# Kernel optimization log

Hardware: AMD Instinct MI355X
Metric: run time of the kernel (lower is better)

Reference implementation:

```python
import jax, jax.numpy as jnp
import numpy as np

B = 256
N = 256


def setup_inputs() -> dict:
    key = jax.random.key(0)
    ks = jax.random.split(key, 6)
    X = jax.random.normal(ks[0], (B, N), dtype=jnp.float32)
    context = jax.random.normal(ks[1], (B, N), dtype=jnp.float32)
    W = jax.random.normal(ks[2], (N, N), dtype=jnp.float32) * 0.1
    scale = jnp.ones((1,), dtype=jnp.float32)
    A = jax.random.uniform(ks[3], (N, N), dtype=jnp.float32)
    cl_weight = jax.random.normal(ks[4], (N * N, N), dtype=jnp.float32) * 0.02
    cl_bias = jax.random.normal(ks[5], (N * N,), dtype=jnp.float32) * 0.02
    t = 3
    return {"X": X, "context": context, "W": W, "scale": scale, "A": A,
            "cl_weight": cl_weight, "cl_bias": cl_bias, "t": t}


def reference(X, context, W, scale, A, cl_weight, cl_bias, t):
    # context_L path: context-conditioned adjustment of W, shape [B, N, N]
    Bsz, n = X.shape
    adjust = (context @ cl_weight.T + cl_bias).reshape(Bsz, n, n)
    W_new = adjust + W  # broadcast [N,N] over batch
    # diag term: sum over rows i of (W_new @ A)[b, i, k] = einsum bij,jk->bk
    d = jnp.einsum('bij,jk->bk', W_new, A)
    eye = jnp.eye(n, dtype=X.dtype)
    L = d[:, :, None] * eye - W_new          # diag_embed(d) - W_new, [B,N,N]
    new_context = context * (t / (t + 1)) + X / (t + 1)
    L_T = scale * jnp.swapaxes(L, -1, -2)    # [B,N,N]
    update = jnp.einsum('bn,bnm->bm', X, L_T)  # matmul(X[...,None,:], L_T).squeeze()
    return (update, new_context)
```

## Files before the change

kernel.cpp:

```cpp
#include <hip/hip_runtime.h>

#define N 256
#define NN 65536

typedef __attribute__((ext_vector_type(8))) __bf16 bf16x8;
typedef __attribute__((ext_vector_type(4))) __bf16 bf16x4v;
typedef __attribute__((ext_vector_type(4))) float f32x4;

#define F_PART   0u
#define F_SPART  2097152u
#define F_WSC    2621440u
#define F_WXCB   2621696u
#define F_SFULL  2687232u
#define F_YADJ   2752768u
#define F_CTXB   2818304u
#define WS_FLOATS 2851072u

static __device__ __forceinline__ f32x4 mfma16(bf16x8 a, bf16x8 b, f32x4 c) {
  return __builtin_amdgcn_mfma_f32_16x16x32_bf16(a, b, c, 0, 0, 0);
}
static __device__ __forceinline__ bf16x4v pack4(float4 v) {
  bf16x4v r;
  r[0] = (__bf16)v.x; r[1] = (__bf16)v.y; r[2] = (__bf16)v.z; r[3] = (__bf16)v.w;
  return r;
}

__global__ void __launch_bounds__(256) kpre(
    const float* __restrict__ X, const float* __restrict__ ctx,
    const float* __restrict__ W, const float* __restrict__ clb,
    const int* __restrict__ tptr, float* __restrict__ out,
    float* __restrict__ ws)
{
  extern __shared__ char smem[];
  const int blk = blockIdx.x;
  const int t = threadIdx.x;
  if (blk < 16) {
    const int b0 = (blk >> 2) * 64;
    const int m0 = (blk & 3) * 64;
    {
      const int row = t >> 2, q = t & 3;
      const int sw = (row & 7) << 4;
      const float4* xp = (const float4*)X + (b0 + row) * 64 + q * 16;
      const float4* wp = (const float4*)W + (m0 + row) * 64 + q * 16;
      const float4* cp = (const float4*)clb + (m0 + row) * 64 + q * 16;
      char* xs = smem;
      char* ps = smem + 32768;
#pragma unroll
      for (int i = 0; i < 16; ++i) {
        float4 xv = xp[i];
        *(bf16x4v*)(xs + row * 512 + ((q * 128 + i * 8) ^ sw)) = pack4(xv);
        float4 wv = wp[i];
        float4 cv = cp[i];
        float4 sv;
        sv.x = wv.x + cv.x; sv.y = wv.y + cv.y;
        sv.z = wv.z + cv.z; sv.w = wv.w + cv.w;
        *(bf16x4v*)(ps + row * 512 + ((q * 128 + i * 8) ^ sw)) = pack4(sv);
      }
    }
    __syncthreads();
    const int lane = t & 63, w = t >> 6;
    const int l15 = lane & 15, lhi = lane >> 4;
    const int wbl = (w >> 1) * 32, wml = (w & 1) * 32;
    const int swz = (l15 & 7) << 4;
    const f32x4 zero = {0.f, 0.f, 0.f, 0.f};
    f32x4 acc[2][2];
    acc[0][0] = zero; acc[0][1] = zero; acc[1][0] = zero; acc[1][1] = zero;
#pragma unroll
    for (int ks = 0; ks < 8; ++ks) {
      const int kb = ks * 64 + lhi * 16;
      bf16x8 a0 = *(const bf16x8*)(smem + (wbl + l15) * 512 + (kb ^ swz));
      bf16x8 a1 = *(const bf16x8*)(smem + (wbl + 16 + l15) * 512 + (kb ^ swz));
      bf16x8 b0 = *(const bf16x8*)(smem + 32768 + (wml + l15) * 512 + (kb ^ swz));
      bf16x8 b1 = *(const bf16x8*)(smem + 32768 + (wml + 16 + l15) * 512 + (kb ^ swz));
      acc[0][0] = mfma16(a0, b0, acc[0][0]);
      acc[0][1] = mfma16(a0, b1, acc[0][1]);
      acc[1][0] = mfma16(a1, b0, acc[1][0]);
      acc[1][1] = mfma16(a1, b1, acc[1][1]);
    }
#pragma unroll
    for (int fb = 0; fb < 2; ++fb)
#pragma unroll
      for (int fm = 0; fm < 2; ++fm)
#pragma unroll
        for (int r = 0; r < 4; ++r) {
          const int b = b0 + wbl + fb * 16 + lhi * 4 + r;
          const int m = m0 + wml + fm * 16 + l15;
          ws[F_WXCB + b * N + m] = acc[fb][fm][r];
        }
  } else if (blk == 16) {
    float sv = 0.f;
    for (int i = 0; i < N; ++i) sv += W[i * N + t] + clb[i * N + t];
    ws[F_WSC + t] = sv;
  } else if (blk < 81) {
    const float tf = (float)(*tptr);
    const float c1 = tf / (tf + 1.f);
    const float c2 = 1.f / (tf + 1.f);
    const int i4 = (blk - 17) * 256 + t;
    const float4 cv = ((const float4*)ctx)[i4];
    const float4 xv = ((const float4*)X)[i4];
    float4 o;
    o.x = cv.x * c1 + xv.x * c2;
    o.y = cv.y * c1 + xv.y * c2;
    o.z = cv.z * c1 + xv.z * c2;
    o.w = cv.w * c1 + xv.w * c2;
    ((float4*)out)[16384 + i4] = o;
  } else {
    const int g = (blk - 81) * 256 + t;
    const float4* p = (const float4*)ctx + g * 2;
    const float4 v0 = p[0], v1 = p[1];
    bf16x8 r;
    r[0] = (__bf16)v0.x; r[1] = (__bf16)v0.y; r[2] = (__bf16)v0.z; r[3] = (__bf16)v0.w;
    r[4] = (__bf16)v1.x; r[5] = (__bf16)v1.y; r[6] = (__bf16)v1.z; r[7] = (__bf16)v1.w;
    ((bf16x8*)(ws + F_CTXB))[g] = r;
  }
}

__global__ void __launch_bounds__(512) kbig(
    const float* __restrict__ X, const float* __restrict__ clw,
    float* __restrict__ ws)
{
  extern __shared__ char smem[];
  char* clws = smem + 131072;
  float* xl = (float*)(smem + 147456);
  const int t = threadIdx.x;
  const int mt = blockIdx.x >> 5;
  const int s = blockIdx.x & 31;
  const int n0 = s * 8;
  const int m0g = mt * 32;
  const float4* clwf4 = (const float4*)clw;

  float4 g0[4];
  int gm[4], gk[4];
#pragma unroll
  for (int i = 0; i < 4; ++i) {
    const int idx = i * 512 + t;
    gm[i] = idx >> 6;
    gk[i] = idx & 63;
    g0[i] = clwf4[(m0g + gm[i]) * 16384 + n0 * 64 + gk[i]];
  }
  {
    const bf16x8* cb = (const bf16x8*)(ws + F_CTXB);
#pragma unroll
    for (int it = 0; it < 16; ++it) {
      const int gg = it * 512 + t;
      bf16x8 v = cb[gg];
      const int row = gg >> 5, c8 = gg & 31;
      *(bf16x8*)(smem + row * 512 + ((c8 * 16) ^ ((row & 7) << 4))) = v;
    }
  }
  if (t < 256) {
    const float4* xp = (const float4*)(X + t * N + n0);
    const float4 x0 = xp[0], x1 = xp[1];
    xl[0 * N + t] = x0.x; xl[1 * N + t] = x0.y; xl[2 * N + t] = x0.z; xl[3 * N + t] = x0.w;
    xl[4 * N + t] = x1.x; xl[5 * N + t] = x1.y; xl[6 * N + t] = x1.z; xl[7 * N + t] = x1.w;
  }
#pragma unroll
  for (int i = 0; i < 4; ++i) {
    *(bf16x4v*)(clws + gm[i] * 512 + ((gk[i] * 8) ^ ((gm[i] & 7) << 4))) = pack4(g0[i]);
  }
  __syncthreads();

  const int lane = t & 63, w = t >> 6;
  const int wb = w * 32, l15 = lane & 15, lhi = lane >> 4;
  const int swz = (l15 & 7) << 4;
  const f32x4 zero = {0.f, 0.f, 0.f, 0.f};
  f32x4 acc[2][2];
  acc[0][0] = zero; acc[0][1] = zero; acc[1][0] = zero; acc[1][1] = zero;

  for (int nn = 0; nn < 8; ++nn) {
    float4 gnx[4];
    if (nn < 7) {
#pragma unroll
      for (int i = 0; i < 4; ++i)
        gnx[i] = clwf4[(m0g + gm[i]) * 16384 + (n0 + nn + 1) * 64 + gk[i]];
    }
    f32x4 h[2][2];
    h[0][0] = zero; h[0][1] = zero; h[1][0] = zero; h[1][1] = zero;
#pragma unroll
    for (int half = 0; half < 2; ++half) {
      bf16x8 af[2][4], bw[2][4];
#pragma unroll
      for (int q = 0; q < 4; ++q) {
        const int kb = half * 256 + q * 64 + lhi * 16;
        af[0][q] = *(const bf16x8*)(smem + (wb + l15) * 512 + (kb ^ swz));
        af[1][q] = *(const bf16x8*)(smem + (wb + 16 + l15) * 512 + (kb ^ swz));
        bw[0][q] = *(const bf16x8*)(clws + (l15) * 512 + (kb ^ swz));
        bw[1][q] = *(const bf16x8*)(clws + (16 + l15) * 512 + (kb ^ swz));
      }
#pragma unroll
      for (int q = 0; q < 4; ++q) {
        h[0][0] = mfma16(af[0][q], bw[0][q], h[0][0]);
        h[0][1] = mfma16(af[0][q], bw[1][q], h[0][1]);
        h[1][0] = mfma16(af[1][q], bw[0][q], h[1][0]);
        h[1][1] = mfma16(af[1][q], bw[1][q], h[1][1]);
      }
    }
    const int ng = n0 + nn;
#pragma unroll
    for (int fb = 0; fb < 2; ++fb) {
      float xv[4];
#pragma unroll
      for (int r = 0; r < 4; ++r)
        xv[r] = xl[nn * N + wb + fb * 16 + lhi * 4 + r];
#pragma unroll
      for (int r = 0; r < 4; ++r) {
        acc[fb][0][r] += xv[r] * h[fb][0][r];
        acc[fb][1][r] += xv[r] * h[fb][1][r];
        float v = h[fb][0][r] + h[fb][1][r];
        v += __shfl_xor(v, 1);
        v += __shfl_xor(v, 2);
        v += __shfl_xor(v, 4);
        v += __shfl_xor(v, 8);
        if (l15 == 0)
          ws[F_SPART + mt * NN + (wb + fb * 16 + lhi * 4 + r) * N + ng] = v;
      }
    }
    __syncthreads();
    if (nn < 7) {
#pragma unroll
      for (int i = 0; i < 4; ++i)
        *(bf16x4v*)(clws + gm[i] * 512 + ((gk[i] * 8) ^ ((gm[i] & 7) << 4))) = pack4(gnx[i]);
    }
    __syncthreads();
  }
  const int base = blockIdx.x * 8192;
#pragma unroll
  for (int fb = 0; fb < 2; ++fb)
#pragma unroll
    for (int fm = 0; fm < 2; ++fm)
#pragma unroll
      for (int r = 0; r < 4; ++r) {
        const int b = wb + fb * 16 + lhi * 4 + r;
        const int ml = fm * 16 + l15;
        ws[F_PART + base + b * 32 + ml] = acc[fb][fm][r];
      }
}

__global__ void __launch_bounds__(256) kred(float* __restrict__ ws)
{
  const int o = blockIdx.x * 256 + threadIdx.x;
  const int b = o >> 8, col = o & 255;
  const int mt = col >> 5, ml = col & 31;
  float y = 0.f;
#pragma unroll
  for (int si = 0; si < 32; ++si)
    y += ws[F_PART + ((mt * 32 + si) * 256 + b) * 32 + ml];
  ws[F_YADJ + o] = y;
  float sv = ws[F_WSC + col];
#pragma unroll
  for (int q = 0; q < 8; ++q)
    sv += ws[F_SPART + q * NN + o];
  ws[F_SFULL + o] = sv;
}

__global__ void __launch_bounds__(256) kfin(
    const float* __restrict__ X, const float* __restrict__ A,
    const float* __restrict__ scale, float* __restrict__ out,
    float* __restrict__ ws)
{
  extern __shared__ char smem[];
  const int t = threadIdx.x, blk = blockIdx.x;
  const int b0 = (blk >> 2) * 64, k0 = (blk & 3) * 64;
  {
    const int row = t >> 2, q = t & 3;
    const int sw = (row & 7) << 4;
    const float4* sp = (const float4*)(ws + F_SFULL + (b0 + row) * N) + q * 16;
#pragma unroll
    for (int i = 0; i < 16; ++i) {
      float4 v = sp[i];
      *(bf16x4v*)(smem + row * 512 + ((q * 128 + i * 8) ^ sw)) = pack4(v);
    }
  }
  {
    const int j = t;
    const float4* ap = (const float4*)(A + j * N + k0);
    char* at = smem + 32768;
#pragma unroll
    for (int i = 0; i < 16; ++i) {
      float4 v = ap[i];
      const int kk = i * 4;
      *(__bf16*)(at + (kk + 0) * 512 + ((j * 2) ^ (((kk + 0) & 7) << 4))) = (__bf16)v.x;
      *(__bf16*)(at + (kk + 1) * 512 + ((j * 2) ^ (((kk + 1) & 7) << 4))) = (__bf16)v.y;
      *(__bf16*)(at + (kk + 2) * 512 + ((j * 2) ^ (((kk + 2) & 7) << 4))) = (__bf16)v.z;
      *(__bf16*)(at + (kk + 3) * 512 + ((j * 2) ^ (((kk + 3) & 7) << 4))) = (__bf16)v.w;
    }
  }
  __syncthreads();
  const int lane = t & 63, w = t >> 6;
  const int l15 = lane & 15, lhi = lane >> 4;
  const int wbl = (w >> 1) * 32, wkl = (w & 1) * 32;
  const int swz = (l15 & 7) << 4;
  const f32x4 zero = {0.f, 0.f, 0.f, 0.f};
  f32x4 acc[2][2];
  acc[0][0] = zero; acc[0][1] = zero; acc[1][0] = zero; acc[1][1] = zero;
#pragma unroll
  for (int ks = 0; ks < 8; ++ks) {
    const int kb = ks * 64 + lhi * 16;
    bf16x8 a0 = *(const bf16x8*)(smem + (wbl + l15) * 512 + (kb ^ swz));
    bf16x8 a1 = *(const bf16x8*)(smem + (wbl + 16 + l15) * 512 + (kb ^ swz));
    bf16x8 b0 = *(const bf16x8*)(smem + 32768 + (wkl + l15) * 512 + (kb ^ swz));
    bf16x8 b1 = *(const bf16x8*)(smem + 32768 + (wkl + 16 + l15) * 512 + (kb ^ swz));
    acc[0][0] = mfma16(a0, b0, acc[0][0]);
    acc[0][1] = mfma16(a0, b1, acc[0][1]);
    acc[1][0] = mfma16(a1, b0, acc[1][0]);
    acc[1][1] = mfma16(a1, b1, acc[1][1]);
  }
  const float sc = scale[0];
#pragma unroll
  for (int fb = 0; fb < 2; ++fb)
#pragma unroll
    for (int fm = 0; fm < 2; ++fm)
#pragma unroll
      for (int r = 0; r < 4; ++r) {
        const int b = b0 + wbl + fb * 16 + lhi * 4 + r;
        const int k = k0 + wkl + fm * 16 + l15;
        const int idx = b * N + k;
        const float d = acc[fb][fm][r];
        out[idx] = sc * (X[idx] * d - ws[F_WXCB + idx] - ws[F_YADJ + idx]);
      }
}

extern "C" void kernel_launch(void* const* d_in, const int* in_sizes, int n_in,
                              void* d_out, int out_size, void* d_ws, size_t ws_size,
                              hipStream_t stream)
{
  const float* X     = (const float*)d_in[0];
  const float* ctx   = (const float*)d_in[1];
  const float* W     = (const float*)d_in[2];
  const float* scale = (const float*)d_in[3];
  const float* A     = (const float*)d_in[4];
  const float* clw   = (const float*)d_in[5];
  const float* clb   = (const float*)d_in[6];
  const int*   tptr  = (const int*)d_in[7];
  float* out = (float*)d_out;
  float* ws  = (float*)d_ws;

  if (ws_size < (size_t)WS_FLOATS * sizeof(float)) return;

  (void)hipFuncSetAttribute((const void*)kpre,
                            hipFuncAttributeMaxDynamicSharedMemorySize, 65536);
  (void)hipFuncSetAttribute((const void*)kbig,
                            hipFuncAttributeMaxDynamicSharedMemorySize, 155648);
  (void)hipFuncSetAttribute((const void*)kfin,
                            hipFuncAttributeMaxDynamicSharedMemorySize, 65536);

  kpre<<<113, 256, 65536, stream>>>(X, ctx, W, clb, tptr, out, ws);
  kbig<<<256, 512, 155648, stream>>>(X, clw, ws);
  kred<<<256, 256, 0, stream>>>(ws);
  kfin<<<16, 256, 65536, stream>>>(X, A, scale, out, ws);
}
```

Before: 61.35 us.

## Remove pre-pass kernel by fusing its work into main and final kernels

Deletes the kpre launch. Its jobs move elsewhere: kbig converts the ctx bf16 A-fragments straight into registers, kfin computes the X·(W+clb)ᵀ product and new_context, and the column sums of W+clb are produced by the mt==0 blocks of kbig. kbig shrinks its shared memory from about 152KB to 56KB by keeping the ctx operand in registers, and it triple-buffers the cl_weight slices with a two-step prefetch, using a single barrier per step. kfin is retiled from 16 to 64 blocks. The intent is to cut launch overhead and the workspace round trip and to raise occupancy, at the cost of more register pressure and redundant ctx loads across blocks.

```diff
diff --git a/kernel.cpp b/kernel.cpp
--- a/kernel.cpp
+++ b/kernel.cpp
@@ -10,11 +10,9 @@
 #define F_PART   0u
 #define F_SPART  2097152u
 #define F_WSC    2621440u
-#define F_WXCB   2621696u
-#define F_SFULL  2687232u
-#define F_YADJ   2752768u
-#define F_CTXB   2818304u
-#define WS_FLOATS 2851072u
+#define F_SFULL  2621696u
+#define F_YADJ   2687232u
+#define WS_FLOATS 2752768u
 
 static __device__ __forceinline__ f32x4 mfma16(bf16x8 a, bf16x8 b, f32x4 c) {
   return __builtin_amdgcn_mfma_f32_16x16x32_bf16(a, b, c, 0, 0, 0);
@@ -24,130 +22,51 @@
   r[0] = (__bf16)v.x; r[1] = (__bf16)v.y; r[2] = (__bf16)v.z; r[3] = (__bf16)v.w;
   return r;
 }
-
-__global__ void __launch_bounds__(256) kpre(
+static __device__ __forceinline__ bf16x8 pack8(float4 a, float4 b) {
+  bf16x8 r;
+  r[0] = (__bf16)a.x; r[1] = (__bf16)a.y; r[2] = (__bf16)a.z; r[3] = (__bf16)a.w;
+  r[4] = (__bf16)b.x; r[5] = (__bf16)b.y; r[6] = (__bf16)b.z; r[7] = (__bf16)b.w;
+  return r;
+}
+
+__global__ void __launch_bounds__(512) kbig(
     const float* __restrict__ X, const float* __restrict__ ctx,
     const float* __restrict__ W, const float* __restrict__ clb,
-    const int* __restrict__ tptr, float* __restrict__ out,
-    float* __restrict__ ws)
+    const float* __restrict__ clw, float* __restrict__ ws)
 {
   extern __shared__ char smem[];
-  const int blk = blockIdx.x;
+  float* xl = (float*)(smem + 49152);
   const int t = threadIdx.x;
-  if (blk < 16) {
-    const int b0 = (blk >> 2) * 64;
-    const int m0 = (blk & 3) * 64;
-    {
-      const int row = t >> 2, q = t & 3;
-      const int sw = (row & 7) << 4;
-      const float4* xp = (const float4*)X + (b0 + row) * 64 + q * 16;
-      const float4* wp = (const float4*)W + (m0 + row) * 64 + q * 16;
-      const float4* cp = (const float4*)clb + (m0 + row) * 64 + q * 16;
-      char* xs = smem;
-      char* ps = smem + 32768;
-#pragma unroll
-      for (int i = 0; i < 16; ++i) {
-        float4 xv = xp[i];
-        *(bf16x4v*)(xs + row * 512 + ((q * 128 + i * 8) ^ sw)) = pack4(xv);
-        float4 wv = wp[i];
-        float4 cv = cp[i];
-        float4 sv;
-        sv.x = wv.x + cv.x; sv.y = wv.y + cv.y;
-        sv.z = wv.z + cv.z; sv.w = wv.w + cv.w;
-        *(bf16x4v*)(ps + row * 512 + ((q * 128 + i * 8) ^ sw)) = pack4(sv);
-      }
-    }
-    __syncthreads();
-    const int lane = t & 63, w = t >> 6;
-    const int l15 = lane & 15, lhi = lane >> 4;
-    const int wbl = (w >> 1) * 32, wml = (w & 1) * 32;
-    const int swz = (l15 & 7) << 4;
-    const f32x4 zero = {0.f, 0.f, 0.f, 0.f};
-    f32x4 acc[2][2];
-    acc[0][0] = zero; acc[0][1] = zero; acc[1][0] = zero; acc[1][1] = zero;
-#pragma unroll
-    for (int ks = 0; ks < 8; ++ks) {
-      const int kb = ks * 64 + lhi * 16;
-      bf16x8 a0 = *(const bf16x8*)(smem + (wbl + l15) * 512 + (kb ^ swz));
-      bf16x8 a1 = *(const bf16x8*)(smem + (wbl + 16 + l15) * 512 + (kb ^ swz));
-      bf16x8 b0 = *(const bf16x8*)(smem + 32768 + (wml + l15) * 512 + (kb ^ swz));
-      bf16x8 b1 = *(const bf16x8*)(smem + 32768 + (wml + 16 + l15) * 512 + (kb ^ swz));
-      acc[0][0] = mfma16(a0, b0, acc[0][0]);
-      acc[0][1] = mfma16(a0, b1, acc[0][1]);
-      acc[1][0] = mfma16(a1, b0, acc[1][0]);
-      acc[1][1] = mfma16(a1, b1, acc[1][1]);
-    }
-#pragma unroll
-    for (int fb = 0; fb < 2; ++fb)
-#pragma unroll
-      for (int fm = 0; fm < 2; ++fm)
-#pragma unroll
-        for (int r = 0; r < 4; ++r) {
-          const int b = b0 + wbl + fb * 16 + lhi * 4 + r;
-          const int m = m0 + wml + fm * 16 + l15;
-          ws[F_WXCB + b * N + m] = acc[fb][fm][r];
-        }
-  } else if (blk == 16) {
-    float sv = 0.f;
-    for (int i = 0; i < N; ++i) sv += W[i * N + t] + clb[i * N + t];
-    ws[F_WSC + t] = sv;
-  } else if (blk < 81) {
-    const float tf = (float)(*tptr);
-    const float c1 = tf / (tf + 1.f);
-    const float c2 = 1.f / (tf + 1.f);
-    const int i4 = (blk - 17) * 256 + t;
-    const float4 cv = ((const float4*)ctx)[i4];
-    const float4 xv = ((const float4*)X)[i4];
-    float4 o;
-    o.x = cv.x * c1 + xv.x * c2;
-    o.y = cv.y * c1 + xv.y * c2;
-    o.z = cv.z * c1 + xv.z * c2;
-    o.w = cv.w * c1 + xv.w * c2;
-    ((float4*)out)[16384 + i4] = o;
-  } else {
-    const int g = (blk - 81) * 256 + t;
-    const float4* p = (const float4*)ctx + g * 2;
-    const float4 v0 = p[0], v1 = p[1];
-    bf16x8 r;
-    r[0] = (__bf16)v0.x; r[1] = (__bf16)v0.y; r[2] = (__bf16)v0.z; r[3] = (__bf16)v0.w;
-    r[4] = (__bf16)v1.x; r[5] = (__bf16)v1.y; r[6] = (__bf16)v1.z; r[7] = (__bf16)v1.w;
-    ((bf16x8*)(ws + F_CTXB))[g] = r;
-  }
-}
-
-__global__ void __launch_bounds__(512) kbig(
-    const float* __restrict__ X, const float* __restrict__ clw,
-    float* __restrict__ ws)
-{
-  extern __shared__ char smem[];
-  char* clws = smem + 131072;
-  float* xl = (float*)(smem + 147456);
-  const int t = threadIdx.x;
-  const int mt = blockIdx.x >> 5;
-  const int s = blockIdx.x & 31;
-  const int n0 = s * 8;
-  const int m0g = mt * 32;
+  const int mt = blockIdx.x >> 5, s = blockIdx.x & 31;
+  const int n0 = s * 8, m0g = mt * 32;
   const float4* clwf4 = (const float4*)clw;
 
-  float4 g0[4];
   int gm[4], gk[4];
+  float4 gA[4], gB[4];
 #pragma unroll
   for (int i = 0; i < 4; ++i) {
     const int idx = i * 512 + t;
-    gm[i] = idx >> 6;
-    gk[i] = idx & 63;
-    g0[i] = clwf4[(m0g + gm[i]) * 16384 + n0 * 64 + gk[i]];
-  }
-  {
-    const bf16x8* cb = (const bf16x8*)(ws + F_CTXB);
-#pragma unroll
-    for (int it = 0; it < 16; ++it) {
-      const int gg = it * 512 + t;
-      bf16x8 v = cb[gg];
-      const int row = gg >> 5, c8 = gg & 31;
-      *(bf16x8*)(smem + row * 512 + ((c8 * 16) ^ ((row & 7) << 4))) = v;
-    }
-  }
+    gm[i] = idx >> 6; gk[i] = idx & 63;
+    gA[i] = clwf4[(m0g + gm[i]) * 16384 + (n0 + 0) * 64 + gk[i]];
+  }
+#pragma unroll
+  for (int i = 0; i < 4; ++i)
+    gB[i] = clwf4[(m0g + gm[i]) * 16384 + (n0 + 1) * 64 + gk[i]];
+
+  const int lane = t & 63, w = t >> 6;
+  const int wb = w * 32, l15 = lane & 15, lhi = lane >> 4;
+  const int swz = (l15 & 7) << 4;
+
+  bf16x8 af[2][8];
+#pragma unroll
+  for (int i = 0; i < 2; ++i)
+#pragma unroll
+    for (int c = 0; c < 8; ++c) {
+      const float4* p =
+          (const float4*)(ctx + (wb + i * 16 + l15) * N + c * 32 + lhi * 8);
+      af[i][c] = pack8(p[0], p[1]);
+    }
+
   if (t < 256) {
     const float4* xp = (const float4*)(X + t * N + n0);
     const float4 x0 = xp[0], x1 = xp[1];
@@ -155,57 +74,48 @@
     xl[4 * N + t] = x1.x; xl[5 * N + t] = x1.y; xl[6 * N + t] = x1.z; xl[7 * N + t] = x1.w;
   }
 #pragma unroll
-  for (int i = 0; i < 4; ++i) {
-    *(bf16x4v*)(clws + gm[i] * 512 + ((gk[i] * 8) ^ ((gm[i] & 7) << 4))) = pack4(g0[i]);
-  }
+  for (int i = 0; i < 4; ++i)
+    *(bf16x4v*)(smem + gm[i] * 512 + ((gk[i] * 8) ^ ((gm[i] & 7) << 4))) = pack4(gA[i]);
   __syncthreads();
 
-  const int lane = t & 63, w = t >> 6;
-  const int wb = w * 32, l15 = lane & 15, lhi = lane >> 4;
-  const int swz = (l15 & 7) << 4;
   const f32x4 zero = {0.f, 0.f, 0.f, 0.f};
   f32x4 acc[2][2];
   acc[0][0] = zero; acc[0][1] = zero; acc[1][0] = zero; acc[1][1] = zero;
 
+#pragma unroll
   for (int nn = 0; nn < 8; ++nn) {
-    float4 gnx[4];
-    if (nn < 7) {
-#pragma unroll
-      for (int i = 0; i < 4; ++i)
-        gnx[i] = clwf4[(m0g + gm[i]) * 16384 + (n0 + nn + 1) * 64 + gk[i]];
-    }
+    if (nn < 6) {
+      if ((nn & 1) == 0) {
+#pragma unroll
+        for (int i = 0; i < 4; ++i)
+          gA[i] = clwf4[(m0g + gm[i]) * 16384 + (n0 + nn + 2) * 64 + gk[i]];
+      } else {
+#pragma unroll
+        for (int i = 0; i < 4; ++i)
+          gB[i] = clwf4[(m0g + gm[i]) * 16384 + (n0 + nn + 2) * 64 + gk[i]];
+      }
+    }
+    char* buf = smem + (nn % 3) * 16384;
     f32x4 h[2][2];
     h[0][0] = zero; h[0][1] = zero; h[1][0] = zero; h[1][1] = zero;
 #pragma unroll
-    for (int half = 0; half < 2; ++half) {
-      bf16x8 af[2][4], bw[2][4];
-#pragma unroll
-      for (int q = 0; q < 4; ++q) {
-        const int kb = half * 256 + q * 64 + lhi * 16;
-        af[0][q] = *(const bf16x8*)(smem + (wb + l15) * 512 + (kb ^ swz));
-        af[1][q] = *(const bf16x8*)(smem + (wb + 16 + l15) * 512 + (kb ^ swz));
-        bw[0][q] = *(const bf16x8*)(clws + (l15) * 512 + (kb ^ swz));
-        bw[1][q] = *(const bf16x8*)(clws + (16 + l15) * 512 + (kb ^ swz));
-      }
-#pragma unroll
-      for (int q = 0; q < 4; ++q) {
-        h[0][0] = mfma16(af[0][q], bw[0][q], h[0][0]);
-        h[0][1] = mfma16(af[0][q], bw[1][q], h[0][1]);
-        h[1][0] = mfma16(af[1][q], bw[0][q], h[1][0]);
-        h[1][1] = mfma16(af[1][q], bw[1][q], h[1][1]);
-      }
+    for (int c = 0; c < 8; ++c) {
+      const int kb = c * 64 + lhi * 16;
+      bf16x8 b0 = *(const bf16x8*)(buf + l15 * 512 + (kb ^ swz));
+      bf16x8 b1 = *(const bf16x8*)(buf + (16 + l15) * 512 + (kb ^ swz));
+      h[0][0] = mfma16(af[0][c], b0, h[0][0]);
+      h[0][1] = mfma16(af[0][c], b1, h[0][1]);
+      h[1][0] = mfma16(af[1][c], b0, h[1][0]);
+      h[1][1] = mfma16(af[1][c], b1, h[1][1]);
     }
     const int ng = n0 + nn;
 #pragma unroll
     for (int fb = 0; fb < 2; ++fb) {
-      float xv[4];
-#pragma unroll
-      for (int r = 0; r < 4; ++r)
-        xv[r] = xl[nn * N + wb + fb * 16 + lhi * 4 + r];
 #pragma unroll
       for (int r = 0; r < 4; ++r) {
-        acc[fb][0][r] += xv[r] * h[fb][0][r];
-        acc[fb][1][r] += xv[r] * h[fb][1][r];
+        const float xv = xl[nn * N + wb + fb * 16 + lhi * 4 + r];
+        acc[fb][0][r] += xv * h[fb][0][r];
+        acc[fb][1][r] += xv * h[fb][1][r];
         float v = h[fb][0][r] + h[fb][1][r];
         v += __shfl_xor(v, 1);
         v += __shfl_xor(v, 2);
@@ -215,25 +125,53 @@
           ws[F_SPART + mt * NN + (wb + fb * 16 + lhi * 4 + r) * N + ng] = v;
       }
     }
+    if (nn < 7) {
+      char* nbuf = smem + ((nn + 1) % 3) * 16384;
+      if (((nn + 1) & 1) == 0) {
+#pragma unroll
+        for (int i = 0; i < 4; ++i)
+          *(bf16x4v*)(nbuf + gm[i] * 512 + ((gk[i] * 8) ^ ((gm[i] & 7) << 4))) = pack4(gA[i]);
+      } else {
+#pragma unroll
+        for (int i = 0; i < 4; ++i)
+          *(bf16x4v*)(nbuf + gm[i] * 512 + ((gk[i] * 8) ^ ((gm[i] & 7) << 4))) = pack4(gB[i]);
+      }
+    }
     __syncthreads();
-    if (nn < 7) {
-#pragma unroll
-      for (int i = 0; i < 4; ++i)
-        *(bf16x4v*)(clws + gm[i] * 512 + ((gk[i] * 8) ^ ((gm[i] & 7) << 4))) = pack4(gnx[i]);
+  }
+  const int base = blockIdx.x * 8192;
+#pragma unroll
+  for (int fb = 0; fb < 2; ++fb)
+#pragma unroll
+    for (int fm = 0; fm < 2; ++fm)
+#pragma unroll
+      for (int r = 0; r < 4; ++r)
+        ws[F_PART + base + (wb + fb * 16 + lhi * 4 + r) * 32 + fm * 16 + l15] =
+            acc[fb][fm][r];
+
+  if (mt == 0) {
+    float* red = xl;
+    if (t < 256) {
+      const float4* wp = (const float4*)(W + t * N + s * 8);
+      const float4* cp = (const float4*)(clb + t * N + s * 8);
+      const float4 a0 = wp[0], a1 = wp[1], b0 = cp[0], b1 = cp[1];
+      red[0 * 256 + t] = a0.x + b0.x; red[1 * 256 + t] = a0.y + b0.y;
+      red[2 * 256 + t] = a0.z + b0.z; red[3 * 256 + t] = a0.w + b0.w;
+      red[4 * 256 + t] = a1.x + b1.x; red[5 * 256 + t] = a1.y + b1.y;
+      red[6 * 256 + t] = a1.z + b1.z; red[7 * 256 + t] = a1.w + b1.w;
     }
     __syncthreads();
-  }
-  const int base = blockIdx.x * 8192;
-#pragma unroll
-  for (int fb = 0; fb < 2; ++fb)
-#pragma unroll
-    for (int fm = 0; fm < 2; ++fm)
-#pragma unroll
-      for (int r = 0; r < 4; ++r) {
-        const int b = wb + fb * 16 + lhi * 4 + r;
-        const int ml = fm * 16 + l15;
-        ws[F_PART + base + b * 32 + ml] = acc[fb][fm][r];
-      }
+    if (t < 64) {
+      const int jj = t >> 3, seg = t & 7;
+      float v = 0.f;
+#pragma unroll
+      for (int i = 0; i < 32; ++i) v += red[jj * 256 + seg * 32 + i];
+      v += __shfl_xor(v, 1);
+      v += __shfl_xor(v, 2);
+      v += __shfl_xor(v, 4);
+      if (seg == 0) ws[F_WSC + s * 8 + jj] = v;
+    }
+  }
 }
 
 __global__ void __launch_bounds__(256) kred(float* __restrict__ ws)
@@ -254,76 +192,80 @@
 }
 
 __global__ void __launch_bounds__(256) kfin(
-    const float* __restrict__ X, const float* __restrict__ A,
-    const float* __restrict__ scale, float* __restrict__ out,
+    const float* __restrict__ X, const float* __restrict__ ctx,
+    const float* __restrict__ W, const float* __restrict__ clb,
+    const float* __restrict__ A, const float* __restrict__ scale,
+    const int* __restrict__ tptr, float* __restrict__ out,
     float* __restrict__ ws)
 {
   extern __shared__ char smem[];
   const int t = threadIdx.x, blk = blockIdx.x;
-  const int b0 = (blk >> 2) * 64, k0 = (blk & 3) * 64;
+  const int b0 = (blk >> 3) * 32, k0 = (blk & 7) * 32;
   {
-    const int row = t >> 2, q = t & 3;
+    const int row = t >> 3, q = t & 7;
     const int sw = (row & 7) << 4;
-    const float4* sp = (const float4*)(ws + F_SFULL + (b0 + row) * N) + q * 16;
-#pragma unroll
-    for (int i = 0; i < 16; ++i) {
-      float4 v = sp[i];
-      *(bf16x4v*)(smem + row * 512 + ((q * 128 + i * 8) ^ sw)) = pack4(v);
-    }
-  }
-  {
-    const int j = t;
-    const float4* ap = (const float4*)(A + j * N + k0);
+    const float4* sp = (const float4*)(ws + F_SFULL + (b0 + row) * N);
+    const float4* xp = (const float4*)(X + (b0 + row) * N);
+    const float4* wp = (const float4*)(W + (k0 + row) * N);
+    const float4* cp = (const float4*)(clb + (k0 + row) * N);
+#pragma unroll
+    for (int i = 0; i < 8; ++i) {
+      const int f4 = q * 8 + i;
+      const int off = row * 512 + ((f4 * 8) ^ sw);
+      *(bf16x4v*)(smem + off) = pack4(sp[f4]);
+      *(bf16x4v*)(smem + 16384 + off) = pack4(xp[f4]);
+      const float4 wv = wp[f4], cv = cp[f4];
+      float4 s2;
+      s2.x = wv.x + cv.x; s2.y = wv.y + cv.y;
+      s2.z = wv.z + cv.z; s2.w = wv.w + cv.w;
+      *(bf16x4v*)(smem + 49152 + off) = pack4(s2);
+    }
+    const float4* ap = (const float4*)(A + t * N + k0);
     char* at = smem + 32768;
 #pragma unroll
-    for (int i = 0; i < 16; ++i) {
-      float4 v = ap[i];
+    for (int i = 0; i < 8; ++i) {
+      const float4 v = ap[i];
       const int kk = i * 4;
-      *(__bf16*)(at + (kk + 0) * 512 + ((j * 2) ^ (((kk + 0) & 7) << 4))) = (__bf16)v.x;
-      *(__bf16*)(at + (kk + 1) * 512 + ((j * 2) ^ (((kk + 1) & 7) << 4))) = (__bf16)v.y;
-      *(__bf16*)(at + (kk + 2) * 512 + ((j * 2) ^ (((kk + 2) & 7) << 4))) = (__bf16)v.z;
-      *(__bf16*)(at + (kk + 3) * 512 + ((j * 2) ^ (((kk + 3) & 7) << 4))) = (__bf16)v.w;
+      *(__bf16*)(at + (kk + 0) * 512 + ((t * 2) ^ (((kk + 0) & 7) << 4))) = (__bf16)v.x;
+      *(__bf16*)(at + (kk + 1) * 512 + ((t * 2) ^ (((kk + 1) & 7) << 4))) = (__bf16)v.y;
+      *(__bf16*)(at + (kk + 2) * 512 + ((t * 2) ^ (((kk + 2) & 7) << 4))) = (__bf16)v.z;
+      *(__bf16*)(at + (kk + 3) * 512 + ((t * 2) ^ (((kk + 3) & 7) << 4))) = (__bf16)v.w;
     }
   }
   __syncthreads();
   const int lane = t & 63, w = t >> 6;
   const int l15 = lane & 15, lhi = lane >> 4;
-  const int wbl = (w >> 1) * 32, wkl = (w & 1) * 32;
+  const int wqb = (w >> 1) * 16, wqk = (w & 1) * 16;
   const int swz = (l15 & 7) << 4;
-  const f32x4 zero = {0.f, 0.f, 0.f, 0.f};
-  f32x4 acc[2][2];
-  acc[0][0] = zero; acc[0][1] = zero; acc[1][0] = zero; acc[1][1] = zero;
-#pragma unroll
-  for (int ks = 0; ks < 8; ++ks) {
-    const int kb = ks * 64 + lhi * 16;
-    bf16x8 a0 = *(const bf16x8*)(smem + (wbl + l15) * 512 + (kb ^ swz));
-    bf16x8 a1 = *(const bf16x8*)(smem + (wbl + 16 + l15) * 512 + (kb ^ swz));
-    bf16x8 b0 = *(const bf16x8*)(smem + 32768 + (wkl + l15) * 512 + (kb ^ swz));
-    bf16x8 b1 = *(const bf16x8*)(smem + 32768 + (wkl + 16 + l15) * 512 + (kb ^ swz));
-    acc[0][0] = mfma16(a0, b0, acc[0][0]);
-    acc[0][1] = mfma16(a0, b1, acc[0][1]);
-    acc[1][0] = mfma16(a1, b0, acc[1][0]);
-    acc[1][1] = mfma16(a1, b1, acc[1][1]);
+  f32x4 accd = {0.f, 0.f, 0.f, 0.f}, accw = {0.f, 0.f, 0.f, 0.f};
+#pragma unroll
+  for (int c = 0; c < 8; ++c) {
+    const int kb = c * 64 + lhi * 16;
+    bf16x8 as  = *(const bf16x8*)(smem + (wqb + l15) * 512 + (kb ^ swz));
+    bf16x8 aat = *(const bf16x8*)(smem + 32768 + (wqk + l15) * 512 + (kb ^ swz));
+    bf16x8 ax  = *(const bf16x8*)(smem + 16384 + (wqb + l15) * 512 + (kb ^ swz));
+    bf16x8 awc = *(const bf16x8*)(smem + 49152 + (wqk + l15) * 512 + (kb ^ swz));
+    accd = mfma16(as, aat, accd);
+    accw = mfma16(ax, awc, accw);
   }
   const float sc = scale[0];
-#pragma unroll
-  for (int fb = 0; fb < 2; ++fb)
-#pragma unroll
-    for (int fm = 0; fm < 2; ++fm)
-#pragma unroll
-      for (int r = 0; r < 4; ++r) {
-        const int b = b0 + wbl + fb * 16 + lhi * 4 + r;
-        const int k = k0 + wkl + fm * 16 + l15;
-        const int idx = b * N + k;
-        const float d = acc[fb][fm][r];
-        out[idx] = sc * (X[idx] * d - ws[F_WXCB + idx] - ws[F_YADJ + idx]);
-      }
+  const float tf = (float)(*tptr);
+  const float c1 = tf / (tf + 1.f), c2 = 1.f / (tf + 1.f);
+#pragma unroll
+  for (int r = 0; r < 4; ++r) {
+    const int b = b0 + wqb + lhi * 4 + r, k = k0 + wqk + l15;
+    const int idx = b * N + k;
+    const float xv = X[idx];
+    out[idx] = sc * (xv * accd[r] - accw[r] - ws[F_YADJ + idx]);
+    out[NN + idx] = ctx[idx] * c1 + xv * c2;
+  }
 }
 
 extern "C" void kernel_launch(void* const* d_in, const int* in_sizes, int n_in,
                               void* d_out, int out_size, void* d_ws, size_t ws_size,
                               hipStream_t stream)
 {
+  (void)in_sizes; (void)n_in; (void)out_size;
   const float* X     = (const float*)d_in[0];
   const float* ctx   = (const float*)d_in[1];
   const float* W     = (const float*)d_in[2];
@@ -337,15 +279,12 @@
 
   if (ws_size < (size_t)WS_FLOATS * sizeof(float)) return;
 
-  (void)hipFuncSetAttribute((const void*)kpre,
-                            hipFuncAttributeMaxDynamicSharedMemorySize, 65536);
   (void)hipFuncSetAttribute((const void*)kbig,
-                            hipFuncAttributeMaxDynamicSharedMemorySize, 155648);
+                            hipFuncAttributeMaxDynamicSharedMemorySize, 57344);
   (void)hipFuncSetAttribute((const void*)kfin,
                             hipFuncAttributeMaxDynamicSharedMemorySize, 65536);
 
-  kpre<<<113, 256, 65536, stream>>>(X, ctx, W, clb, tptr, out, ws);
-  kbig<<<256, 512, 155648, stream>>>(X, clw, ws);
+  kbig<<<256, 512, 57344, stream>>>(X, ctx, W, clb, clw, ws);
   kred<<<256, 256, 0, stream>>>(ws);
-  kfin<<<16, 256, 65536, stream>>>(X, A, scale, out, ws);
-}
+  kfin<<<64, 256, 65536, stream>>>(X, ctx, W, clb, A, scale, tptr, out, ws);
+}
```

New measurement: 55.61 us. 9.4% less time.
